# Kernel optimization log

Measured on AMD Instinct MI355X. Metric: run time of the kernel, lower is better.

Reference implementation:

```python
import jax, jax.numpy as jnp
import numpy as np
from jax import lax

NUM_SEGMENTS = 50
HIDDEN = 128
IN_CH = 64
LOGSIG_DIM = IN_CH + IN_CH * (IN_CH - 1) // 2 + IN_CH  # level1 + Levy area + startpoint


def setup_inputs() -> dict:
    key = jax.random.key(0)
    k0, k1, k2, k3, k4 = jax.random.split(key, 5)
    B, C, T, V = 16, IN_CH, 200, 25
    x = jax.random.normal(k0, (B, C, T, V), dtype=jnp.float32)
    s = 1.0 / np.sqrt(HIDDEN).astype(np.float32)
    W_ih = jax.random.uniform(k1, (4 * HIDDEN, LOGSIG_DIM), jnp.float32, -s, s)
    W_hh = jax.random.uniform(k2, (4 * HIDDEN, HIDDEN), jnp.float32, -s, s)
    b_ih = jax.random.uniform(k3, (4 * HIDDEN,), jnp.float32, -s, s)
    b_hh = jax.random.uniform(k4, (4 * HIDDEN,), jnp.float32, -s, s)
    return {"x": x, "W_ih": W_ih, "W_hh": W_hh, "b_ih": b_ih, "b_hh": b_hh}


def _segment_logsig(xn):
    # xn: (N, C, T). Split T into NUM_SEGMENTS chunks; level-2 log-signature per chunk.
    N, C, T = xn.shape
    L = T // NUM_SEGMENTS  # points per segment
    p = xn.transpose(0, 2, 1).reshape(N, NUM_SEGMENTS, L, C)  # path points
    start = p[:, :, 0]                                  # (N,S,C) segment startpoint
    inc = p[:, :, 1:] - p[:, :, :-1]                    # (N,S,L-1,C) increments
    dev = p[:, :, :-1] - start[:, :, None]              # (N,S,L-1,C) p_t - p_0
    # Level-2 iterated integrals (cross terms): S2_ij = sum_t dev_t,i * inc_t,j
    S2 = jnp.einsum('nsti,nstj->nsij', dev, inc)        # (N,S,C,C)
    A = 0.5 * (S2 - S2.transpose(0, 1, 3, 2))           # Levy area (antisymmetric part)
    iu, ju = jnp.triu_indices(C, k=1)
    levy = A[:, :, iu, ju]                              # (N,S,C(C-1)/2)
    lvl1 = p[:, :, -1] - start                          # (N,S,C) level-1 term
    return jnp.concatenate([lvl1, levy, start], axis=-1)  # (N,S,LOGSIG_DIM)


def _lstm(seq, W_ih, W_hh, b_ih, b_hh):
    # seq: (N, S, F). Single-layer unidirectional LSTM, torch gate order (i,f,g,o).
    N = seq.shape[0]
    x_proj = jnp.einsum('nsf,gf->nsg', seq, W_ih) + b_ih + b_hh  # (N,S,4H)

    def step(carry, xt):
        h, c = carry
        gates = xt + h @ W_hh.T
        i, f, g, o = jnp.split(gates, 4, axis=-1)
        c = jax.nn.sigmoid(f) * c + jax.nn.sigmoid(i) * jnp.tanh(g)
        h = jax.nn.sigmoid(o) * jnp.tanh(c)
        return (h, c), h

    h0 = jnp.zeros((N, HIDDEN), seq.dtype)
    c0 = jnp.zeros((N, HIDDEN), seq.dtype)
    _, hs = lax.scan(step, (h0, c0), x_proj.transpose(1, 0, 2))
    return hs.transpose(1, 0, 2)  # (N,S,H)


def reference(x, W_ih, W_hh, b_ih, b_hh):
    B, C, T, V = x.shape
    xn = x.transpose(0, 3, 1, 2).reshape(B * V, C, T)
    ls = _segment_logsig(xn)                      # (B*V, S, LOGSIG_DIM)
    h = _lstm(ls, W_ih, W_hh, b_ih, b_hh)          # (B*V, S, H)
    out = h.reshape(B, V, NUM_SEGMENTS, HIDDEN).transpose(0, 3, 2, 1)
    return out  # (B, H, S, V)
```

## Files before the change

### kernel.cpp

```cpp
#include <hip/hip_runtime.h>
#include <stdint.h>

#define NSEG 50
#define HID 128
#define KDIM 2144
#define KD2 2176
#define KD2B 4352
#define NROW 20000
#define NROW_PAD 20096
#define GATES 512
#define NSEQ 400

typedef __attribute__((ext_vector_type(8))) _Float16 f16x8;
typedef __attribute__((ext_vector_type(4))) float f32x4;
typedef __attribute__((ext_vector_type(4))) uint32_t u32x4;

#define GLB_SPACE __attribute__((address_space(1)))
#define LDS_SPACE __attribute__((address_space(3)))

__device__ __forceinline__ void g2lds16(const void* g, void* l) {
    __builtin_amdgcn_global_load_lds((const GLB_SPACE uint32_t*)g,
                                     (LDS_SPACE uint32_t*)l, 16, 0, 0);
}

__global__ __launch_bounds__(256) void prep_kernel(const float* __restrict__ Wih,
                                                   const float* __restrict__ Whh,
                                                   const float* __restrict__ bih,
                                                   const float* __restrict__ bhh,
                                                   _Float16* __restrict__ wh,
                                                   _Float16* __restrict__ whh16,
                                                   float* __restrict__ bias) {
    int idx = blockIdx.x * 256 + threadIdx.x;
    const int nwih = 512 * KD2;
    const int nwhh = 512 * HID;
    if (idx < nwih) {
        int row = idx / KD2;
        int k = idx - row * KD2;
        wh[idx] = (k < KDIM) ? (_Float16)Wih[row * KDIM + k] : (_Float16)0.0f;
    } else if (idx < nwih + nwhh) {
        int q = idx - nwih;
        whh16[q] = (_Float16)Whh[q];
    } else if (idx < nwih + nwhh + 512) {
        int g = idx - nwih - nwhh;
        bias[g] = bih[g] + bhh[g];
    }
}

__global__ __launch_bounds__(256) void feat_kernel(const float* __restrict__ x,
                                                   _Float16* __restrict__ feat) {
    int bid = blockIdx.x;
    int b = bid / NSEG;
    int s = bid - b * NSEG;
    int tid = threadIdx.x;

    __shared__ float pbuf[64 * 100];
    __shared__ float2 uu[25 * 64];
    __shared__ float2 vvb[25 * 64];

    for (int i = tid; i < 6400; i += 256) {
        int c = i / 100;
        int r = i - c * 100;
        pbuf[c * 100 + r] = x[(((size_t)b * 64 + c) * 200 + 4 * s) * 25 + r];
    }
    if (tid < 800) {
        int v = tid >> 5;
        int k = 2144 + (tid & 31);
        size_t m = ((size_t)(b * 25 + v)) * NSEG + s;
        feat[m * KD2 + k] = (_Float16)0.0f;
    }
    __syncthreads();

    for (int i = tid; i < 1600; i += 256) {
        int v = i >> 6;
        int c = i & 63;
        float p0 = pbuf[c * 100 + v];
        float p1 = pbuf[c * 100 + 25 + v];
        float p2 = pbuf[c * 100 + 50 + v];
        float p3 = pbuf[c * 100 + 75 + v];
        uu[v * 64 + c] = make_float2(p1 - p0, p2 - p0);
        vvb[v * 64 + c] = make_float2(p2 - p1, p3 - p2);
        size_t m = ((size_t)(b * 25 + v)) * NSEG + s;
        feat[m * KD2 + c] = (_Float16)(p3 - p0);
        feat[m * KD2 + 2080 + c] = (_Float16)p0;
    }
    __syncthreads();

    for (int ch = 0; ch < 8; ch++) {
        int pidx = ch * 256 + tid;
        if (pidx < 2016) {
            float disc = 16129.0f - 8.0f * (float)pidx;
            int i = (int)((127.0f - sqrtf(disc)) * 0.5f);
            int off = 63 * i - (i * (i - 1)) / 2;
            while (off > pidx) { i--; off = 63 * i - (i * (i - 1)) / 2; }
            while (63 * (i + 1) - ((i + 1) * i) / 2 <= pidx) { i++; off = 63 * i - (i * (i - 1)) / 2; }
            int j = pidx - off + i + 1;
            int k = 64 + pidx;
            for (int v = 0; v < 25; v++) {
                float2 ui = uu[v * 64 + i], uj = uu[v * 64 + j];
                float2 vi = vvb[v * 64 + i], vj = vvb[v * 64 + j];
                float val = 0.5f * (ui.x * vj.x - uj.x * vi.x + ui.y * vj.y - uj.y * vi.y);
                size_t m = ((size_t)(b * 25 + v)) * NSEG + s;
                feat[m * KD2 + k] = (_Float16)val;
            }
        }
    }
}

__global__ __launch_bounds__(256, 3) void gemm_kernel(const _Float16* __restrict__ feat,
                                                      const _Float16* __restrict__ wh,
                                                      const float* __restrict__ bias,
                                                      _Float16* __restrict__ xproj2) {
    int bid = blockIdx.x;
    int x = bid & 7;
    int t = bid >> 3;
    int nb = t & 3;
    int mt = (t >> 2) * 8 + x;
    if (mt >= 157) return;
    int m0 = mt * 128;
    int n0 = nb * 128;
    int tid = threadIdx.x;
    int wave = tid >> 6;
    int lane = tid & 63;
    int quad = lane >> 4;
    int l15 = lane & 15;
    int wm = (wave & 1) * 64;
    int wn = (wave >> 1) * 64;

    int r8 = lane >> 3;
    int gcol = ((lane & 7) * 16) ^ (r8 * 16);

    __shared__ __align__(16) _Float16 smem[16896];
    char* As = (char*)smem;
    char* Bs = (char*)smem + 128 * 128;

    const f32x4 z4 = {0.f, 0.f, 0.f, 0.f};
    f32x4 acc[4][4];
    for (int i = 0; i < 4; i++)
        for (int j = 0; j < 4; j++) acc[i][j] = z4;

    const char* featB = (const char*)feat;
    const char* whB = (const char*)wh;

    for (int kt = 0; kt < 34; kt++) {
        size_t kb = (size_t)kt * 128;
        __syncthreads();
        for (int it = 0; it < 4; it++) {
            int rb = it * 32 + wave * 8;
            g2lds16(featB + (size_t)(m0 + rb + r8) * KD2B + kb + gcol, As + rb * 128);
            g2lds16(whB + (size_t)(n0 + rb + r8) * KD2B + kb + gcol, Bs + rb * 128);
        }
        __syncthreads();

        for (int ks = 0; ks < 2; ks++) {
            int off = ((ks * 64) | (quad * 16)) ^ ((l15 & 7) * 16);
            f16x8 af[4], bf[4];
            for (int tt = 0; tt < 4; tt++) {
                af[tt] = *(const f16x8*)(As + (wm + tt * 16 + l15) * 128 + off);
                bf[tt] = *(const f16x8*)(Bs + (wn + tt * 16 + l15) * 128 + off);
            }
            for (int mtl = 0; mtl < 4; mtl++)
                for (int ntl = 0; ntl < 4; ntl++)
                    acc[mtl][ntl] = __builtin_amdgcn_mfma_f32_16x16x32_f16(af[mtl], bf[ntl], acc[mtl][ntl], 0, 0, 0);
        }
    }

    __syncthreads();
    for (int ntl = 0; ntl < 4; ntl++) {
        int nl = wn + ntl * 16 + l15;
        float bv = bias[n0 + nl];
        for (int mtl = 0; mtl < 4; mtl++)
            for (int r = 0; r < 4; r++) {
                int ml = wm + mtl * 16 + quad * 4 + r;
                smem[ml * 132 + nl] = (_Float16)(acc[mtl][ntl][r] + bv);
            }
    }
    __syncthreads();
    {
        int row = tid >> 1;
        int seg = tid & 1;
        int m = m0 + row;
        if (m < NROW) {
            unsigned q = (unsigned)m / 50u;
            unsigned s = (unsigned)m - q * 50u;
            const char* src = (const char*)smem + row * 264 + seg * 128;
            char* dst = (char*)xproj2 + ((size_t)s * NSEQ + q) * 1024 + (size_t)n0 * 2 + seg * 128;
            for (int i = 0; i < 8; i++)
                *(u32x4*)(dst + i * 16) = *(const u32x4*)(src + i * 16);
        }
    }
}

__global__ __launch_bounds__(256, 1) void lstm_kernel(const _Float16* __restrict__ xproj2,
                                                      const _Float16* __restrict__ whh,
                                                      _Float16* __restrict__ hseq) {
    int bid = blockIdx.x;
    int tid = threadIdx.x;
    int wave = tid >> 6;
    int lane = tid & 63;
    int quad = lane >> 4;
    int col = lane & 15;
    int hh = quad >> 1;
    int sq4 = (quad & 1) * 4;
    int hid = wave * 32 + hh * 16 + col;

    __shared__ __align__(16) char xbuf[2 * 8 * 1040];
    __shared__ __align__(16) _Float16 hbuf[2][8 * 136];

    f16x8 bfrag[8][4];
    for (int ntl = 0; ntl < 8; ntl++) {
        int g = ntl >> 1, h2 = ntl & 1;
        int n = g * 128 + wave * 32 + h2 * 16 + col;
        for (int kq = 0; kq < 4; kq++)
            bfrag[ntl][kq] = *(const f16x8*)(whh + (size_t)n * HID + kq * 32 + quad * 8);
    }
    for (int i = tid; i < 2 * 8 * 136; i += 256) ((_Float16*)hbuf)[i] = (_Float16)0.0f;
    float cst[4] = {0.f, 0.f, 0.f, 0.f};
    _Float16 hprev[4];

    const char* xsrc = (const char*)xproj2;
    {
        size_t base = (size_t)(bid * 8) * 1024;
        g2lds16(xsrc + base + (size_t)wave * 1024 + lane * 16, xbuf + wave * 1040);
        g2lds16(xsrc + base + (size_t)(wave + 4) * 1024 + lane * 16, xbuf + (wave + 4) * 1040);
    }
    __syncthreads();

    const f32x4 z4 = {0.f, 0.f, 0.f, 0.f};
    for (int s = 0; s < NSEG; s++) {
        int cur = s & 1;
        int nxt = cur ^ 1;

        if (s > 0) {
            for (int r = 0; r < 4; r++)
                hseq[((size_t)(s - 1) * NSEQ + bid * 8 + sq4 + r) * HID + hid] = hprev[r];
        }
        if (s + 1 < NSEG) {
            size_t base = ((size_t)(s + 1) * NSEQ + bid * 8) * 1024;
            g2lds16(xsrc + base + (size_t)wave * 1024 + lane * 16,
                    xbuf + nxt * 8320 + wave * 1040);
            g2lds16(xsrc + base + (size_t)(wave + 4) * 1024 + lane * 16,
                    xbuf + nxt * 8320 + (wave + 4) * 1040);
        }

        f16x8 afrag[4];
        for (int kq = 0; kq < 4; kq++)
            afrag[kq] = *(const f16x8*)(&hbuf[cur][(col & 7) * 136 + kq * 32 + quad * 8]);

        float xp[4][4];
        for (int g = 0; g < 4; g++) {
            int gc = g * 128 + hid;
            for (int r = 0; r < 4; r++)
                xp[g][r] = (float)(*(const _Float16*)(xbuf + cur * 8320 +
                               (sq4 + r) * 1040 + gc * 2));
        }

        f32x4 acc[8];
        for (int ntl = 0; ntl < 8; ntl++) {
            acc[ntl] = z4;
            for (int kq = 0; kq < 4; kq++)
                acc[ntl] = __builtin_amdgcn_mfma_f32_16x16x32_f16(afrag[kq], bfrag[ntl][kq], acc[ntl], 0, 0, 0);
        }

        f32x4 ai = hh ? acc[1] : acc[0];
        f32x4 af_ = hh ? acc[3] : acc[2];
        f32x4 ag = hh ? acc[5] : acc[4];
        f32x4 ao = hh ? acc[7] : acc[6];

        for (int r = 0; r < 4; r++) {
            float ip = ai[r] + xp[0][r];
            float fp = af_[r] + xp[1][r];
            float gp = ag[r] + xp[2][r];
            float op = ao[r] + xp[3][r];
            float si = __fdividef(1.0f, 1.0f + __expf(-ip));
            float sf = __fdividef(1.0f, 1.0f + __expf(-fp));
            float so = __fdividef(1.0f, 1.0f + __expf(-op));
            float eg = __expf(-2.0f * gp);
            float tg = __fdividef(1.0f - eg, 1.0f + eg);
            cst[r] = sf * cst[r] + si * tg;
            float ec = __expf(-2.0f * cst[r]);
            float tc = __fdividef(1.0f - ec, 1.0f + ec);
            float hv = so * tc;
            hprev[r] = (_Float16)hv;
            hbuf[nxt][(sq4 + r) * 136 + hid] = hprev[r];
        }
        __syncthreads();
    }
    for (int r = 0; r < 4; r++)
        hseq[((size_t)(NSEG - 1) * NSEQ + bid * 8 + sq4 + r) * HID + hid] = hprev[r];
}

__global__ __launch_bounds__(256) void tr_kernel(const _Float16* __restrict__ hseq,
                                                 float* __restrict__ out) {
    int bid = blockIdx.x;
    int b = bid / NSEG;
    int s = bid - b * NSEG;
    int tid = threadIdx.x;

    __shared__ _Float16 buf[25 * 130];

    const uint32_t* src32 = (const uint32_t*)(hseq + ((size_t)s * NSEQ + b * 25) * HID);
    uint32_t* buf32 = (uint32_t*)buf;
    for (int i = tid; i < 1600; i += 256) {
        int v = i >> 6;
        int d = i & 63;
        buf32[v * 65 + d] = src32[i];
    }
    __syncthreads();
    for (int i = tid; i < 3200; i += 256) {
        int hid = i / 25;
        int v = i - hid * 25;
        out[(((size_t)b * 128 + hid) * NSEG + s) * 25 + v] = (float)buf[v * 130 + hid];
    }
}

extern "C" void kernel_launch(void* const* d_in, const int* in_sizes, int n_in,
                              void* d_out, int out_size, void* d_ws, size_t ws_size,
                              hipStream_t stream) {
    const float* x = (const float*)d_in[0];
    const float* Wih = (const float*)d_in[1];
    const float* Whh = (const float*)d_in[2];
    const float* bih = (const float*)d_in[3];
    const float* bhh = (const float*)d_in[4];
    float* out = (float*)d_out;

    char* ws = (char*)d_ws;
    size_t off = 0;
    _Float16* feat = (_Float16*)(ws + off);   off += (size_t)NROW_PAD * KD2 * 2;
    _Float16* xproj2 = (_Float16*)(ws + off); off += (size_t)NSEG * NSEQ * GATES * 2;
    _Float16* hseq = (_Float16*)(ws + off);   off += (size_t)NSEG * NSEQ * HID * 2;
    _Float16* wh = (_Float16*)(ws + off);     off += (size_t)512 * KD2 * 2;
    _Float16* whh16 = (_Float16*)(ws + off);  off += (size_t)512 * HID * 2;
    float* bias = (float*)(ws + off);         off += 512 * 4;

    int prep_total = 512 * KD2 + 512 * HID + 512;
    hipLaunchKernelGGL(prep_kernel, dim3((prep_total + 255) / 256), dim3(256), 0, stream,
                       Wih, Whh, bih, bhh, wh, whh16, bias);
    hipLaunchKernelGGL(feat_kernel, dim3(16 * NSEG), dim3(256), 0, stream, x, feat);
    hipLaunchKernelGGL(gemm_kernel, dim3(640), dim3(256), 0, stream, feat, wh, bias, xproj2);
    hipLaunchKernelGGL(lstm_kernel, dim3(50), dim3(256), 0, stream, xproj2, whh16, hseq);
    hipLaunchKernelGGL(tr_kernel, dim3(16 * NSEG), dim3(256), 0, stream, hseq, out);
}
```

Before: 258.1 us.

## Split LSTM recurrence into 100 blocks of 4 sequences with 8 waves

The LSTM kernel now processes 4 sequences per block across 8 waves, each wave owning 16 hidden units, launched as 100 blocks of 512 threads instead of 50 blocks of 256. The per-step critical path shrinks: each wave issues 16 MFMAs instead of 32 and each thread runs one gate nonlinearity instead of four. This targets the serial 50-step latency of the recurrence. In exchange, most MFMA rows are wasted, since only 4 of 16 A rows are real sequences, and the barrier now synchronizes 8 waves.

```diff
diff --git a/kernel.cpp b/kernel.cpp
--- a/kernel.cpp
+++ b/kernel.cpp
@@ -190,7 +190,7 @@
     }
 }
 
-__global__ __launch_bounds__(256, 1) void lstm_kernel(const _Float16* __restrict__ xproj2,
+__global__ __launch_bounds__(512, 2) void lstm_kernel(const _Float16* __restrict__ xproj2,
                                                       const _Float16* __restrict__ whh,
                                                       _Float16* __restrict__ hseq) {
     int bid = blockIdx.x;
@@ -199,30 +199,24 @@
     int lane = tid & 63;
     int quad = lane >> 4;
     int col = lane & 15;
-    int hh = quad >> 1;
-    int sq4 = (quad & 1) * 4;
-    int hid = wave * 32 + hh * 16 + col;
-
-    __shared__ __align__(16) char xbuf[2 * 8 * 1040];
-    __shared__ __align__(16) _Float16 hbuf[2][8 * 136];
-
-    f16x8 bfrag[8][4];
-    for (int ntl = 0; ntl < 8; ntl++) {
-        int g = ntl >> 1, h2 = ntl & 1;
-        int n = g * 128 + wave * 32 + h2 * 16 + col;
+    int hid = wave * 16 + col;
+
+    __shared__ __align__(16) char xbuf[2 * 4 * 1040];
+    __shared__ __align__(16) _Float16 hbuf[2][4 * 136];
+
+    f16x8 bfrag[4][4];
+    for (int g = 0; g < 4; g++) {
+        int n = g * 128 + hid;
         for (int kq = 0; kq < 4; kq++)
-            bfrag[ntl][kq] = *(const f16x8*)(whh + (size_t)n * HID + kq * 32 + quad * 8);
-    }
-    for (int i = tid; i < 2 * 8 * 136; i += 256) ((_Float16*)hbuf)[i] = (_Float16)0.0f;
-    float cst[4] = {0.f, 0.f, 0.f, 0.f};
-    _Float16 hprev[4];
+            bfrag[g][kq] = *(const f16x8*)(whh + (size_t)n * HID + kq * 32 + quad * 8);
+    }
+    for (int i = tid; i < 2 * 4 * 136; i += 512) ((_Float16*)hbuf)[i] = (_Float16)0.0f;
+    float cst = 0.0f;
+    _Float16 hprev = (_Float16)0.0f;
 
     const char* xsrc = (const char*)xproj2;
-    {
-        size_t base = (size_t)(bid * 8) * 1024;
-        g2lds16(xsrc + base + (size_t)wave * 1024 + lane * 16, xbuf + wave * 1040);
-        g2lds16(xsrc + base + (size_t)(wave + 4) * 1024 + lane * 16, xbuf + (wave + 4) * 1040);
-    }
+    if (wave < 4)
+        g2lds16(xsrc + (size_t)(bid * 4 + wave) * 1024 + lane * 16, xbuf + wave * 1040);
     __syncthreads();
 
     const f32x4 z4 = {0.f, 0.f, 0.f, 0.f};
@@ -230,63 +224,53 @@
         int cur = s & 1;
         int nxt = cur ^ 1;
 
-        if (s > 0) {
-            for (int r = 0; r < 4; r++)
-                hseq[((size_t)(s - 1) * NSEQ + bid * 8 + sq4 + r) * HID + hid] = hprev[r];
-        }
-        if (s + 1 < NSEG) {
-            size_t base = ((size_t)(s + 1) * NSEQ + bid * 8) * 1024;
-            g2lds16(xsrc + base + (size_t)wave * 1024 + lane * 16,
-                    xbuf + nxt * 8320 + wave * 1040);
-            g2lds16(xsrc + base + (size_t)(wave + 4) * 1024 + lane * 16,
-                    xbuf + nxt * 8320 + (wave + 4) * 1040);
-        }
+        if (s > 0)
+            hseq[((size_t)(s - 1) * NSEQ + bid * 4 + quad) * HID + hid] = hprev;
+        if (s + 1 < NSEG && wave < 4)
+            g2lds16(xsrc + ((size_t)(s + 1) * NSEQ + bid * 4 + wave) * 1024 + lane * 16,
+                    xbuf + nxt * 4160 + wave * 1040);
 
         f16x8 afrag[4];
         for (int kq = 0; kq < 4; kq++)
-            afrag[kq] = *(const f16x8*)(&hbuf[cur][(col & 7) * 136 + kq * 32 + quad * 8]);
-
-        float xp[4][4];
+            afrag[kq] = *(const f16x8*)(&hbuf[cur][(col & 3) * 136 + kq * 32 + quad * 8]);
+
+        float xp[4];
+        for (int g = 0; g < 4; g++)
+            xp[g] = (float)(*(const _Float16*)(xbuf + cur * 4160 +
+                           quad * 1040 + (g * 128 + hid) * 2));
+
+        f32x4 acc[4];
         for (int g = 0; g < 4; g++) {
-            int gc = g * 128 + hid;
-            for (int r = 0; r < 4; r++)
-                xp[g][r] = (float)(*(const _Float16*)(xbuf + cur * 8320 +
-                               (sq4 + r) * 1040 + gc * 2));
-        }
-
-        f32x4 acc[8];
-        for (int ntl = 0; ntl < 8; ntl++) {
-            acc[ntl] = z4;
+            acc[g] = z4;
             for (int kq = 0; kq < 4; kq++)
-                acc[ntl] = __builtin_amdgcn_mfma_f32_16x16x32_f16(afrag[kq], bfrag[ntl][kq], acc[ntl], 0, 0, 0);
-        }
-
-        f32x4 ai = hh ? acc[1] : acc[0];
-        f32x4 af_ = hh ? acc[3] : acc[2];
-        f32x4 ag = hh ? acc[5] : acc[4];
-        f32x4 ao = hh ? acc[7] : acc[6];
-
-        for (int r = 0; r < 4; r++) {
-            float ip = ai[r] + xp[0][r];
-            float fp = af_[r] + xp[1][r];
-            float gp = ag[r] + xp[2][r];
-            float op = ao[r] + xp[3][r];
-            float si = __fdividef(1.0f, 1.0f + __expf(-ip));
-            float sf = __fdividef(1.0f, 1.0f + __expf(-fp));
-            float so = __fdividef(1.0f, 1.0f + __expf(-op));
-            float eg = __expf(-2.0f * gp);
-            float tg = __fdividef(1.0f - eg, 1.0f + eg);
-            cst[r] = sf * cst[r] + si * tg;
-            float ec = __expf(-2.0f * cst[r]);
-            float tc = __fdividef(1.0f - ec, 1.0f + ec);
-            float hv = so * tc;
-            hprev[r] = (_Float16)hv;
-            hbuf[nxt][(sq4 + r) * 136 + hid] = hprev[r];
-        }
+                acc[g] = __builtin_amdgcn_mfma_f32_16x16x32_f16(afrag[kq], bfrag[g][kq], acc[g], 0, 0, 0);
+        }
+
+        float gv[4];
+        for (int g = 0; g < 4; g++) {
+            float lo = (quad & 1) ? acc[g][1] : acc[g][0];
+            float hi = (quad & 1) ? acc[g][3] : acc[g][2];
+            gv[g] = (quad & 2) ? hi : lo;
+        }
+
+        float ip = gv[0] + xp[0];
+        float fp = gv[1] + xp[1];
+        float gp = gv[2] + xp[2];
+        float op = gv[3] + xp[3];
+        float si = __fdividef(1.0f, 1.0f + __expf(-ip));
+        float sf = __fdividef(1.0f, 1.0f + __expf(-fp));
+        float so = __fdividef(1.0f, 1.0f + __expf(-op));
+        float eg = __expf(-2.0f * gp);
+        float tg = __fdividef(1.0f - eg, 1.0f + eg);
+        cst = sf * cst + si * tg;
+        float ec = __expf(-2.0f * cst);
+        float tc = __fdividef(1.0f - ec, 1.0f + ec);
+        float hv = so * tc;
+        hprev = (_Float16)hv;
+        hbuf[nxt][quad * 136 + hid] = hprev;
         __syncthreads();
     }
-    for (int r = 0; r < 4; r++)
-        hseq[((size_t)(NSEG - 1) * NSEQ + bid * 8 + sq4 + r) * HID + hid] = hprev[r];
+    hseq[((size_t)(NSEG - 1) * NSEQ + bid * 4 + quad) * HID + hid] = hprev;
 }
 
 __global__ __launch_bounds__(256) void tr_kernel(const _Float16* __restrict__ hseq,
@@ -337,6 +321,6 @@
                        Wih, Whh, bih, bhh, wh, whh16, bias);
     hipLaunchKernelGGL(feat_kernel, dim3(16 * NSEG), dim3(256), 0, stream, x, feat);
     hipLaunchKernelGGL(gemm_kernel, dim3(640), dim3(256), 0, stream, feat, wh, bias, xproj2);
-    hipLaunchKernelGGL(lstm_kernel, dim3(50), dim3(256), 0, stream, xproj2, whh16, hseq);
+    hipLaunchKernelGGL(lstm_kernel, dim3(100), dim3(512), 0, stream, xproj2, whh16, hseq);
     hipLaunchKernelGGL(tr_kernel, dim3(16 * NSEG), dim3(256), 0, stream, hseq, out);
 }
```

Measured after the change: 225.5 us. -12.6%, faster.
